# Kernel optimization log

Hardware: AMD Instinct MI355X
Metric: run time of the kernel (lower is better)

Reference implementation:

```python
import jax, jax.numpy as jnp
import numpy as np

B = 4096      # batch
OBS = 512     # observation dim
T = 10        # num_tasks
E = 8         # num_experts
W = 1024      # width
H = 12        # head_dim
EPS = 1e-8


def setup_inputs() -> dict:
    key = jax.random.key(0)
    ks = jax.random.split(key, 8)
    obs = jax.random.normal(ks[0], (B, OBS), jnp.float32)
    task_id = jax.random.randint(ks[1], (B,), 0, T)
    task_onehot = jax.nn.one_hot(task_id, T, dtype=jnp.float32)
    x = jnp.concatenate([obs, task_onehot], axis=-1)  # (B, OBS+T)
    he = lambda k, shape, fan: jax.random.normal(k, shape, jnp.float32) * np.float32(np.sqrt(2.0 / fan))
    te_W = he(ks[2], (T, E), T)               # task-embedding Dense (no bias)
    W0 = he(ks[3], (E, OBS, W), OBS); b0 = jnp.zeros((E, W), jnp.float32)
    W1 = he(ks[4], (E, W, W), W);     b1 = jnp.zeros((E, W), jnp.float32)
    W2 = he(ks[5], (E, W, W), W);     b2 = jnp.zeros((E, W), jnp.float32)
    head_W = he(ks[6], (T, W, H), W); head_b = jnp.zeros((T, H), jnp.float32)
    return dict(x=x, te_W=te_W, W0=W0, b0=b0, W1=W1, b1=b1, W2=W2, b2=b2,
                head_W=head_W, head_b=head_b)


def _gram_schmidt(eo):
    # eo: (B, E, W) -> orthonormal basis (B, E, W), sequential over expert axis
    basis = [eo[:, 0] / (jnp.linalg.norm(eo[:, 0], axis=1, keepdims=True) + EPS)]
    for i in range(1, E):
        Bm = jnp.stack(basis, axis=1)               # (B, i, W)
        v = eo[:, i]                                # (B, W)
        coeff = jnp.einsum('bd,bid->bi', v, Bm)     # projections onto current basis
        w = v - jnp.einsum('bi,bid->bd', coeff, Bm)
        basis.append(w / (jnp.linalg.norm(w, axis=1, keepdims=True) + EPS))
    return jnp.stack(basis, axis=1)


def reference(x, te_W, W0, b0, W1, b1, W2, b2, head_W, head_b):
    task_oh = x[:, -T:]                              # (B, T) one-hot
    obs = x[:, :-T]                                  # (B, OBS)
    te = task_oh @ te_W                              # (B, E) task embedding
    # per-expert MLP (vmapped over experts via stacked weights)
    h = jax.nn.relu(jnp.einsum('bd,edw->bew', obs, W0) + b0)
    h = jax.nn.relu(jnp.einsum('bew,ewv->bev', h, W1) + b1)
    eo = jnp.einsum('bew,ewv->bev', h, W2) + b2      # (B, E, W)
    basis = _gram_schmidt(eo)                        # (B, E, W)
    feat = jnp.tanh(jnp.einsum('bek,be->bk', basis, te))  # (B, W)
    heads = jnp.einsum('bk,tkh->bth', feat, head_W) + head_b  # (B, T, H)
    idx = jnp.argmax(task_oh, axis=-1)
    return heads[jnp.arange(x.shape[0]), idx]        # (B, H)
```

## Files before the change

### kernel.cpp

```cpp
#include <hip/hip_runtime.h>
#include <stdint.h>

#define B_SZ   4096
#define OBS    512
#define T_TASKS 10
#define E_EXP  8
#define W_DIM  1024
#define H_OUT  12
#define XROW   522
#define NTOT   8192

using f32x4  = __attribute__((ext_vector_type(4))) float;
using bf16x8 = __attribute__((ext_vector_type(8))) short;

__device__ __forceinline__ unsigned short f2bf(float f) {
  union { float f; unsigned u; } x; x.f = f;
  unsigned r = x.u + 0x7FFF + ((x.u >> 16) & 1);
  return (unsigned short)(r >> 16);
}
__device__ __forceinline__ float bf2f(unsigned short h) {
  union { unsigned u; float f; } x; x.u = ((unsigned)h) << 16;
  return x.f;
}

__device__ __forceinline__ void gload_lds16(const void* g, void* l) {
  __builtin_amdgcn_global_load_lds(
      (const __attribute__((address_space(1))) void*)g,
      (__attribute__((address_space(3))) void*)l,
      16, 0, 0);
}


__global__ void k_obs_bf16(const float* __restrict__ x, unsigned short* __restrict__ obsB) {
  int i = blockIdx.x * 256 + threadIdx.x;
  int b = i >> 9, c = i & 511;
  obsB[i] = f2bf(x[(size_t)b * XROW + c]);
}

__global__ void k_wt(const float* __restrict__ Wsrc, unsigned short* __restrict__ Wt, int K) {
  __shared__ float tile[32][33];
  int e  = blockIdx.z;
  int n0 = blockIdx.x * 32, k0 = blockIdx.y * 32;
  const float* Ws = Wsrc + (size_t)e * K * W_DIM;
  unsigned short* Wd = Wt + (size_t)e * W_DIM * K;
  int tx = threadIdx.x & 31, ty = threadIdx.x >> 5;
#pragma unroll
  for (int r = 0; r < 4; ++r)
    tile[ty + r * 8][tx] = Ws[(size_t)(k0 + ty + r * 8) * W_DIM + n0 + tx];
  __syncthreads();
#pragma unroll
  for (int r = 0; r < 4; ++r)
    Wd[(size_t)(n0 + ty + r * 8) * K + k0 + tx] = f2bf(tile[tx][ty + r * 8]);
}


template <bool RELU>
__global__ __launch_bounds__(512, 2) void k_gemm256(
    const unsigned short* __restrict__ A, int lda, int aExpStride,
    const unsigned short* __restrict__ Bt, int K,
    const float* __restrict__ bias,
    unsigned short* __restrict__ C)
{
  extern __shared__ char lds[];
  const int tid  = threadIdx.x;
  const int lane = tid & 63, wid = tid >> 6;
  const int wm = wid >> 2, wn = wid & 3;
  const int rlo = lane & 15, kg = lane >> 4;

  int bid = blockIdx.x;
  int xcd = bid & 7, loc = bid >> 3;
  int mblk = ((xcd & 1) << 3) | (loc & 7);
  int nblk = ((xcd >> 1) << 3) | (loc >> 3);
  int m0 = mblk * 256, n0g = nblk * 256;
  int e = n0g >> 10, n0e = n0g & 1023;

  const unsigned short* Ab = A + (size_t)e * aExpStride;
  const unsigned short* Bb = Bt + ((size_t)e * 1024 + n0e) * (size_t)K;

  const int idx0 = tid, idx1 = 512 + tid;
  const int r0 = idx0 >> 3, p0 = idx0 & 7, c0 = p0 ^ (r0 & 7);
  const int r1 = idx1 >> 3, p1 = idx1 & 7, c1 = p1 ^ (r1 & 7);

  const int NT = K >> 6;
  const size_t ldaz = (size_t)lda, ldkz = (size_t)K;

  auto stageA = [&](int buf, int h, int kt) {
    const unsigned short* g0 = Ab + (size_t)(m0 + h * 128 + r0) * ldaz + kt * 64 + c0 * 8;
    const unsigned short* g1 = Ab + (size_t)(m0 + h * 128 + r1) * ldaz + kt * 64 + c1 * 8;
    char* l = lds + buf * 65536 + h * 16384;
    gload_lds16(g0, l + idx0 * 16);
    gload_lds16(g1, l + idx1 * 16);
  };
  auto stageB = [&](int buf, int h, int kt) {
    const unsigned short* g0 = Bb + (size_t)(h * 128 + r0) * ldkz + kt * 64 + c0 * 8;
    const unsigned short* g1 = Bb + (size_t)(h * 128 + r1) * ldkz + kt * 64 + c1 * 8;
    char* l = lds + buf * 65536 + 32768 + h * 16384;
    gload_lds16(g0, l + idx0 * 16);
    gload_lds16(g1, l + idx1 * 16);
  };
  auto rdA = [&](int buf, int mh, int mi, int ks) -> bf16x8 {
    int r = mi * 32 + wm * 16 + rlo;
    int p = (ks * 4 + kg) ^ (r & 7);
    return *(const bf16x8*)(lds + buf * 65536 + mh * 16384 + r * 128 + p * 16);
  };
  auto rdB = [&](int buf, int nh, int ni, int ks) -> bf16x8 {
    int r = ni * 64 + wn * 16 + rlo;
    int p = (ks * 4 + kg) ^ (r & 7);
    return *(const bf16x8*)(lds + buf * 65536 + 32768 + nh * 16384 + r * 128 + p * 16);
  };

  f32x4 acc[8][4];
#pragma unroll
  for (int i = 0; i < 8; ++i)
#pragma unroll
    for (int j = 0; j < 4; ++j) acc[i][j] = f32x4{0.f, 0.f, 0.f, 0.f};

  bf16x8 af[8], b0f[4], b1f[4];

  stageA(0, 0, 0); stageB(0, 0, 0); stageB(0, 1, 0); stageA(0, 1, 0);
  asm volatile("s_waitcnt vmcnt(4)" ::: "memory");
  __builtin_amdgcn_sched_barrier(0);
  asm volatile("s_barrier" ::: "memory");

  for (int t = 0; t < NT; ++t) {
    int buf = t & 1, nbuf = buf ^ 1, tn = t + 1;
    bool st = tn < NT;

#pragma unroll
    for (int mi = 0; mi < 4; ++mi)
#pragma unroll
      for (int ks = 0; ks < 2; ++ks) af[mi * 2 + ks] = rdA(buf, 0, mi, ks);
#pragma unroll
    for (int ni = 0; ni < 2; ++ni)
#pragma unroll
      for (int ks = 0; ks < 2; ++ks) b0f[ni * 2 + ks] = rdB(buf, 0, ni, ks);
    if (st) stageA(nbuf, 0, tn);
    asm volatile("s_waitcnt vmcnt(4)" ::: "memory");
    __builtin_amdgcn_sched_barrier(0);
    asm volatile("s_barrier" ::: "memory");
    asm volatile("s_waitcnt lgkmcnt(0)" ::: "memory");
    __builtin_amdgcn_sched_barrier(0);
    __builtin_amdgcn_s_setprio(1);
#pragma unroll
    for (int ks = 0; ks < 2; ++ks)
#pragma unroll
      for (int mi = 0; mi < 4; ++mi)
#pragma unroll
        for (int ni = 0; ni < 2; ++ni)
          acc[mi][ni] = __builtin_amdgcn_mfma_f32_16x16x32_bf16(af[mi * 2 + ks], b0f[ni * 2 + ks], acc[mi][ni], 0, 0, 0);
    __builtin_amdgcn_s_setprio(0);
    __builtin_amdgcn_sched_barrier(0);
    asm volatile("s_barrier" ::: "memory");

#pragma unroll
    for (int ni = 0; ni < 2; ++ni)
#pragma unroll
      for (int ks = 0; ks < 2; ++ks) b1f[ni * 2 + ks] = rdB(buf, 1, ni, ks);
    if (st) stageB(nbuf, 0, tn);
    asm volatile("s_waitcnt vmcnt(4)" ::: "memory");
    __builtin_amdgcn_sched_barrier(0);
    asm volatile("s_barrier" ::: "memory");
    asm volatile("s_waitcnt lgkmcnt(0)" ::: "memory");
    __builtin_amdgcn_sched_barrier(0);
    __builtin_amdgcn_s_setprio(1);
#pragma unroll
    for (int ks = 0; ks < 2; ++ks)
#pragma unroll
      for (int mi = 0; mi < 4; ++mi)
#pragma unroll
        for (int ni = 0; ni < 2; ++ni)
          acc[mi][2 + ni] = __builtin_amdgcn_mfma_f32_16x16x32_bf16(af[mi * 2 + ks], b1f[ni * 2 + ks], acc[mi][2 + ni], 0, 0, 0);
    __builtin_amdgcn_s_setprio(0);
    __builtin_amdgcn_sched_barrier(0);
    asm volatile("s_barrier" ::: "memory");

#pragma unroll
    for (int mi = 0; mi < 4; ++mi)
#pragma unroll
      for (int ks = 0; ks < 2; ++ks) af[mi * 2 + ks] = rdA(buf, 1, mi, ks);
    if (st) stageB(nbuf, 1, tn);
    __builtin_amdgcn_sched_barrier(0);
    asm volatile("s_barrier" ::: "memory");
    asm volatile("s_waitcnt lgkmcnt(0)" ::: "memory");
    __builtin_amdgcn_sched_barrier(0);
    __builtin_amdgcn_s_setprio(1);
#pragma unroll
    for (int ks = 0; ks < 2; ++ks)
#pragma unroll
      for (int mi = 0; mi < 4; ++mi)
#pragma unroll
        for (int ni = 0; ni < 2; ++ni)
          acc[4 + mi][2 + ni] = __builtin_amdgcn_mfma_f32_16x16x32_bf16(af[mi * 2 + ks], b1f[ni * 2 + ks], acc[4 + mi][2 + ni], 0, 0, 0);
    __builtin_amdgcn_s_setprio(0);
    __builtin_amdgcn_sched_barrier(0);
    asm volatile("s_barrier" ::: "memory");

    if (st) stageA(nbuf, 1, tn);
    asm volatile("s_waitcnt vmcnt(4)" ::: "memory");
    __builtin_amdgcn_sched_barrier(0);
    asm volatile("s_barrier" ::: "memory");
    __builtin_amdgcn_s_setprio(1);
#pragma unroll
    for (int ks = 0; ks < 2; ++ks)
#pragma unroll
      for (int mi = 0; mi < 4; ++mi)
#pragma unroll
        for (int ni = 0; ni < 2; ++ni)
          acc[4 + mi][ni] = __builtin_amdgcn_mfma_f32_16x16x32_bf16(af[mi * 2 + ks], b0f[ni * 2 + ks], acc[4 + mi][ni], 0, 0, 0);
    __builtin_amdgcn_s_setprio(0);
    __builtin_amdgcn_sched_barrier(0);
    asm volatile("s_barrier" ::: "memory");
  }

  int rbase = kg * 4;
#pragma unroll
  for (int fi = 0; fi < 8; ++fi) {
    int mh = fi >> 2, mi = fi & 3;
    int rowg = m0 + mh * 128 + mi * 32 + wm * 16 + rbase;
#pragma unroll
    for (int fj = 0; fj < 4; ++fj) {
      int nh = fj >> 1, ni = fj & 1;
      int colr = nh * 128 + ni * 64 + wn * 16 + rlo;
      int colg = n0g + colr;
      float bv = bias[e * W_DIM + n0e + colr];
#pragma unroll
      for (int j = 0; j < 4; ++j) {
        float v = acc[fi][fj][j] + bv;
        if (RELU) v = fmaxf(v, 0.0f);
        C[(size_t)(rowg + j) * NTOT + colg] = f2bf(v);
      }
    }
  }
}


__device__ __forceinline__ float wred(float s) {
#pragma unroll
  for (int m = 32; m; m >>= 1) s += __shfl_xor(s, m, 64);
  return s;
}

__global__ __launch_bounds__(256, 1) void k_gs_wave(
    const unsigned short* __restrict__ eo,
    const float* __restrict__ x,
    const float* __restrict__ te_W,
    const float* __restrict__ head_W,
    const float* __restrict__ head_b,
    float* __restrict__ out)
{
  int wid = threadIdx.x >> 6, lane = threadIdx.x & 63;
  int b = blockIdx.x * 4 + wid;

  float v[8][16];
  const unsigned short* row = eo + (size_t)b * NTOT;
#pragma unroll
  for (int i = 0; i < E_EXP; ++i) {
#pragma unroll
    for (int half = 0; half < 2; ++half) {
      bf16x8 t = *(const bf16x8*)&row[i * 1024 + half * 512 + lane * 8];
#pragma unroll
      for (int k = 0; k < 8; ++k) v[i][half * 8 + k] = bf2f((unsigned short)t[k]);
    }
  }

  int idx = 0; float mv = x[(size_t)b * XROW + OBS];
#pragma unroll
  for (int t = 1; t < T_TASKS; ++t) {
    float val = x[(size_t)b * XROW + OBS + t];
    if (val > mv) { mv = val; idx = t; }
  }

  float cf[7];
#pragma unroll
  for (int i = 0; i < E_EXP; ++i) {
#pragma unroll
    for (int j = 0; j < 7; ++j) {
      if (j < i) {
        float p = 0.f;
#pragma unroll
        for (int c = 0; c < 16; ++c) p += v[i][c] * v[j][c];
        cf[j] = wred(p);
      }
    }
#pragma unroll
    for (int c = 0; c < 16; ++c) {
      float w = v[i][c];
#pragma unroll
      for (int j = 0; j < 7; ++j)
        if (j < i) w -= cf[j] * v[j][c];
      v[i][c] = w;
    }
    float p = 0.f;
#pragma unroll
    for (int c = 0; c < 16; ++c) p += v[i][c] * v[i][c];
    float nrm = sqrtf(wred(p));
    float s = 1.0f / (nrm + 1e-8f);
#pragma unroll
    for (int c = 0; c < 16; ++c) v[i][c] *= s;
  }

  float te[E_EXP];
#pragma unroll
  for (int e2 = 0; e2 < E_EXP; ++e2) te[e2] = te_W[idx * E_EXP + e2];

  float ph[H_OUT];
#pragma unroll
  for (int h = 0; h < H_OUT; ++h) ph[h] = 0.f;
  const float* hw = head_W + (size_t)idx * W_DIM * H_OUT;

#pragma unroll
  for (int half = 0; half < 2; ++half) {
#pragma unroll
    for (int k = 0; k < 8; ++k) {
      int c = half * 512 + lane * 8 + k;
      float f = 0.f;
#pragma unroll
      for (int e2 = 0; e2 < E_EXP; ++e2) f += te[e2] * v[e2][half * 8 + k];
      f = tanhf(f);
      const float* hwc = hw + (size_t)c * H_OUT;
#pragma unroll
      for (int h = 0; h < H_OUT; ++h) ph[h] += f * hwc[h];
    }
  }

#pragma unroll
  for (int h = 0; h < H_OUT; ++h) ph[h] = wred(ph[h]);
  if (lane == 0) {
#pragma unroll
    for (int h = 0; h < H_OUT; ++h)
      out[(size_t)b * H_OUT + h] = ph[h] + head_b[idx * H_OUT + h];
  }
}


extern "C" void kernel_launch(void* const* d_in, const int* in_sizes, int n_in,
                              void* d_out, int out_size, void* d_ws, size_t ws_size,
                              hipStream_t stream) {
  const float* x     = (const float*)d_in[0];
  const float* te_W  = (const float*)d_in[1];
  const float* W0    = (const float*)d_in[2];
  const float* b0    = (const float*)d_in[3];
  const float* W1    = (const float*)d_in[4];
  const float* b1    = (const float*)d_in[5];
  const float* W2    = (const float*)d_in[6];
  const float* b2    = (const float*)d_in[7];
  const float* headW = (const float*)d_in[8];
  const float* headb = (const float*)d_in[9];
  float* out = (float*)d_out;

  char* ws = (char*)d_ws;
  size_t off = 0;
  auto alloc = [&](size_t bytes) {
    void* p = ws + off;
    off += (bytes + 255) & ~(size_t)255;
    return p;
  };
  unsigned short* obsB = (unsigned short*)alloc((size_t)B_SZ * OBS * 2);
  unsigned short* W0t  = (unsigned short*)alloc((size_t)8 * 1024 * 512 * 2);
  unsigned short* W1t  = (unsigned short*)alloc((size_t)8 * 1024 * 1024 * 2);
  unsigned short* W2t  = (unsigned short*)alloc((size_t)8 * 1024 * 1024 * 2);
  unsigned short* h0   = (unsigned short*)alloc((size_t)B_SZ * NTOT * 2);
  unsigned short* h1   = (unsigned short*)alloc((size_t)B_SZ * NTOT * 2);
  unsigned short* eo   = (unsigned short*)alloc((size_t)B_SZ * NTOT * 2);
  (void)ws_size; (void)in_sizes; (void)n_in; (void)out_size;

  k_obs_bf16<<<(B_SZ * OBS) / 256, 256, 0, stream>>>(x, obsB);
  k_wt<<<dim3(32, 16, 8), 256, 0, stream>>>(W0, W0t, 512);
  k_wt<<<dim3(32, 32, 8), 256, 0, stream>>>(W1, W1t, 1024);
  k_wt<<<dim3(32, 32, 8), 256, 0, stream>>>(W2, W2t, 1024);

  k_gemm256<true ><<<512, 512, 131072, stream>>>(obsB, 512,  0,    W0t, 512,  b0, h0);
  k_gemm256<true ><<<512, 512, 131072, stream>>>(h0,   NTOT, 1024, W1t, 1024, b1, h1);
  k_gemm256<false><<<512, 512, 131072, stream>>>(h1,   NTOT, 1024, W2t, 1024, b2, eo);

  k_gs_wave<<<B_SZ / 4, 256, 0, stream>>>(eo, x, te_W, headW, headb, out);
}
```

Baseline: 261.4 us.

## Restructure GEMM main loop to prefetch next tile's fragments and drop barriers

Reorganises the ping-pong GEMM main loop so A/B register fragments for the next iteration are read from LDS at the end of the current one, and the A half-0 tile is staged two iterations ahead into the buffer just consumed. Each phase now uses a single barrier instead of two, and the explicit lgkmcnt waits are dropped. Out-of-range stages are clamped to reload the last tile rather than skipped. The aim is to overlap LDS reads and global loads with MFMA work and cut synchronisation stalls. In exchange the vmcnt accounting becomes more delicate and the clamped stages issue redundant loads.

Result: faster. 245.3 us (-6.2%).

```diff
diff --git a/kernel.cpp b/kernel.cpp
--- a/kernel.cpp
+++ b/kernel.cpp
@@ -29,6 +29,12 @@
       (__attribute__((address_space(3))) void*)l,
       16, 0, 0);
 }
+
+#define VMCNT4  do { asm volatile("s_waitcnt vmcnt(4)" ::: "memory"); \
+                     __builtin_amdgcn_sched_barrier(0); } while (0)
+#define BARRIER do { asm volatile("s_barrier" ::: "memory"); \
+                     __builtin_amdgcn_sched_barrier(0); } while (0)
+#define SCHED0  __builtin_amdgcn_sched_barrier(0)
 
 
 __global__ void k_obs_bf16(const float* __restrict__ x, unsigned short* __restrict__ obsB) {
@@ -115,101 +121,102 @@
 #pragma unroll
     for (int j = 0; j < 4; ++j) acc[i][j] = f32x4{0.f, 0.f, 0.f, 0.f};
 
-  bf16x8 af[8], b0f[4], b1f[4];
+  bf16x8 af[8], bf0[4], bf1[4];
 
   stageA(0, 0, 0); stageB(0, 0, 0); stageB(0, 1, 0); stageA(0, 1, 0);
-  asm volatile("s_waitcnt vmcnt(4)" ::: "memory");
-  __builtin_amdgcn_sched_barrier(0);
-  asm volatile("s_barrier" ::: "memory");
+  stageA(1, 0, (1 < NT - 1) ? 1 : NT - 1);
+  asm volatile("s_waitcnt vmcnt(6)" ::: "memory");
+  SCHED0;
+  BARRIER;
+#pragma unroll
+  for (int mi = 0; mi < 4; ++mi)
+#pragma unroll
+    for (int ks = 0; ks < 2; ++ks) af[mi * 2 + ks] = rdA(0, 0, mi, ks);
+#pragma unroll
+  for (int ni = 0; ni < 2; ++ni)
+#pragma unroll
+    for (int ks = 0; ks < 2; ++ks) bf0[ni * 2 + ks] = rdB(0, 0, ni, ks);
 
   for (int t = 0; t < NT; ++t) {
-    int buf = t & 1, nbuf = buf ^ 1, tn = t + 1;
-    bool st = tn < NT;
-
+    int buf = t & 1, nbuf = buf ^ 1;
+    int tn  = (t + 1 < NT) ? t + 1 : NT - 1;
+    int tn2 = (t + 2 < NT) ? t + 2 : NT - 1;
+
+    VMCNT4;
+    BARRIER;
+#pragma unroll
+    for (int ni = 0; ni < 2; ++ni)
+#pragma unroll
+      for (int ks = 0; ks < 2; ++ks) bf1[ni * 2 + ks] = rdB(buf, 1, ni, ks);
+    stageB(nbuf, 0, tn);
+    SCHED0;
+    __builtin_amdgcn_s_setprio(1);
+#pragma unroll
+    for (int ks = 0; ks < 2; ++ks)
+#pragma unroll
+      for (int mi = 0; mi < 4; ++mi)
+#pragma unroll
+        for (int ni = 0; ni < 2; ++ni)
+          acc[mi][ni] = __builtin_amdgcn_mfma_f32_16x16x32_bf16(af[mi * 2 + ks], bf0[ni * 2 + ks], acc[mi][ni], 0, 0, 0);
+    __builtin_amdgcn_s_setprio(0);
+    SCHED0;
+
+    VMCNT4;
+    BARRIER;
+    stageB(nbuf, 1, tn);
+    SCHED0;
+    __builtin_amdgcn_s_setprio(1);
+#pragma unroll
+    for (int ks = 0; ks < 2; ++ks)
+#pragma unroll
+      for (int mi = 0; mi < 4; ++mi)
+#pragma unroll
+        for (int ni = 0; ni < 2; ++ni)
+          acc[mi][2 + ni] = __builtin_amdgcn_mfma_f32_16x16x32_bf16(af[mi * 2 + ks], bf1[ni * 2 + ks], acc[mi][2 + ni], 0, 0, 0);
+    __builtin_amdgcn_s_setprio(0);
+    SCHED0;
 #pragma unroll
     for (int mi = 0; mi < 4; ++mi)
 #pragma unroll
-      for (int ks = 0; ks < 2; ++ks) af[mi * 2 + ks] = rdA(buf, 0, mi, ks);
+      for (int ks = 0; ks < 2; ++ks) af[mi * 2 + ks] = rdA(buf, 1, mi, ks);
+
+    VMCNT4;
+    BARRIER;
+    stageA(nbuf, 1, tn);
+    SCHED0;
+    __builtin_amdgcn_s_setprio(1);
+#pragma unroll
+    for (int ks = 0; ks < 2; ++ks)
+#pragma unroll
+      for (int mi = 0; mi < 4; ++mi)
+#pragma unroll
+        for (int ni = 0; ni < 2; ++ni)
+          acc[4 + mi][2 + ni] = __builtin_amdgcn_mfma_f32_16x16x32_bf16(af[mi * 2 + ks], bf1[ni * 2 + ks], acc[4 + mi][2 + ni], 0, 0, 0);
+    __builtin_amdgcn_s_setprio(0);
+    SCHED0;
+
+    VMCNT4;
+    BARRIER;
+    stageA(buf, 0, tn2);
+    SCHED0;
+    __builtin_amdgcn_s_setprio(1);
+#pragma unroll
+    for (int ks = 0; ks < 2; ++ks)
+#pragma unroll
+      for (int mi = 0; mi < 4; ++mi)
+#pragma unroll
+        for (int ni = 0; ni < 2; ++ni)
+          acc[4 + mi][ni] = __builtin_amdgcn_mfma_f32_16x16x32_bf16(af[mi * 2 + ks], bf0[ni * 2 + ks], acc[4 + mi][ni], 0, 0, 0);
+    __builtin_amdgcn_s_setprio(0);
+    SCHED0;
+#pragma unroll
+    for (int mi = 0; mi < 4; ++mi)
+#pragma unroll
+      for (int ks = 0; ks < 2; ++ks) af[mi * 2 + ks] = rdA(nbuf, 0, mi, ks);
 #pragma unroll
     for (int ni = 0; ni < 2; ++ni)
 #pragma unroll
-      for (int ks = 0; ks < 2; ++ks) b0f[ni * 2 + ks] = rdB(buf, 0, ni, ks);
-    if (st) stageA(nbuf, 0, tn);
-    asm volatile("s_waitcnt vmcnt(4)" ::: "memory");
-    __builtin_amdgcn_sched_barrier(0);
-    asm volatile("s_barrier" ::: "memory");
-    asm volatile("s_waitcnt lgkmcnt(0)" ::: "memory");
-    __builtin_amdgcn_sched_barrier(0);
-    __builtin_amdgcn_s_setprio(1);
-#pragma unroll
-    for (int ks = 0; ks < 2; ++ks)
-#pragma unroll
-      for (int mi = 0; mi < 4; ++mi)
-#pragma unroll
-        for (int ni = 0; ni < 2; ++ni)
-          acc[mi][ni] = __builtin_amdgcn_mfma_f32_16x16x32_bf16(af[mi * 2 + ks], b0f[ni * 2 + ks], acc[mi][ni], 0, 0, 0);
-    __builtin_amdgcn_s_setprio(0);
-    __builtin_amdgcn_sched_barrier(0);
-    asm volatile("s_barrier" ::: "memory");
-
-#pragma unroll
-    for (int ni = 0; ni < 2; ++ni)
-#pragma unroll
-      for (int ks = 0; ks < 2; ++ks) b1f[ni * 2 + ks] = rdB(buf, 1, ni, ks);
-    if (st) stageB(nbuf, 0, tn);
-    asm volatile("s_waitcnt vmcnt(4)" ::: "memory");
-    __builtin_amdgcn_sched_barrier(0);
-    asm volatile("s_barrier" ::: "memory");
-    asm volatile("s_waitcnt lgkmcnt(0)" ::: "memory");
-    __builtin_amdgcn_sched_barrier(0);
-    __builtin_amdgcn_s_setprio(1);
-#pragma unroll
-    for (int ks = 0; ks < 2; ++ks)
-#pragma unroll
-      for (int mi = 0; mi < 4; ++mi)
-#pragma unroll
-        for (int ni = 0; ni < 2; ++ni)
-          acc[mi][2 + ni] = __builtin_amdgcn_mfma_f32_16x16x32_bf16(af[mi * 2 + ks], b1f[ni * 2 + ks], acc[mi][2 + ni], 0, 0, 0);
-    __builtin_amdgcn_s_setprio(0);
-    __builtin_amdgcn_sched_barrier(0);
-    asm volatile("s_barrier" ::: "memory");
-
-#pragma unroll
-    for (int mi = 0; mi < 4; ++mi)
-#pragma unroll
-      for (int ks = 0; ks < 2; ++ks) af[mi * 2 + ks] = rdA(buf, 1, mi, ks);
-    if (st) stageB(nbuf, 1, tn);
-    __builtin_amdgcn_sched_barrier(0);
-    asm volatile("s_barrier" ::: "memory");
-    asm volatile("s_waitcnt lgkmcnt(0)" ::: "memory");
-    __builtin_amdgcn_sched_barrier(0);
-    __builtin_amdgcn_s_setprio(1);
-#pragma unroll
-    for (int ks = 0; ks < 2; ++ks)
-#pragma unroll
-      for (int mi = 0; mi < 4; ++mi)
-#pragma unroll
-        for (int ni = 0; ni < 2; ++ni)
-          acc[4 + mi][2 + ni] = __builtin_amdgcn_mfma_f32_16x16x32_bf16(af[mi * 2 + ks], b1f[ni * 2 + ks], acc[4 + mi][2 + ni], 0, 0, 0);
-    __builtin_amdgcn_s_setprio(0);
-    __builtin_amdgcn_sched_barrier(0);
-    asm volatile("s_barrier" ::: "memory");
-
-    if (st) stageA(nbuf, 1, tn);
-    asm volatile("s_waitcnt vmcnt(4)" ::: "memory");
-    __builtin_amdgcn_sched_barrier(0);
-    asm volatile("s_barrier" ::: "memory");
-    __builtin_amdgcn_s_setprio(1);
-#pragma unroll
-    for (int ks = 0; ks < 2; ++ks)
-#pragma unroll
-      for (int mi = 0; mi < 4; ++mi)
-#pragma unroll
-        for (int ni = 0; ni < 2; ++ni)
-          acc[4 + mi][ni] = __builtin_amdgcn_mfma_f32_16x16x32_bf16(af[mi * 2 + ks], b0f[ni * 2 + ks], acc[4 + mi][ni], 0, 0, 0);
-    __builtin_amdgcn_s_setprio(0);
-    __builtin_amdgcn_sched_barrier(0);
-    asm volatile("s_barrier" ::: "memory");
+      for (int ks = 0; ks < 2; ++ks) bf0[ni * 2 + ks] = rdB(nbuf, 0, ni, ks);
   }
 
   int rbase = kg * 4;
```
